# Performance work log

Measured on AMD Instinct MI355X. Metric: run time of the kernel, lower is better.

Reference implementation:

```python
import jax, jax.numpy as jnp
import numpy as np

N_NODES = 50000
N_EDGES = 800000
IN_FEATS = 9
H_FEATS = 64
HEADS = 3
N_CLASSES = 2
NEG_SLOPE = 0.2  # DGL GATConv default leaky_relu slope


def _gat_layer(x, src, dst, W, attn_l, attn_r, bias, n_nodes):
    """One DGL-style GATConv: returns [N, H, F_out] (pre head-sum)."""
    H, Fo = attn_l.shape
    feat = (x @ W).reshape(n_nodes, H, Fo)            # [N,H,Fo]
    el = jnp.einsum('nhf,hf->nh', feat, attn_l)        # [N,H]
    er = jnp.einsum('nhf,hf->nh', feat, attn_r)        # [N,H]
    e = jax.nn.leaky_relu(el[src] + er[dst], negative_slope=NEG_SLOPE)  # [E,H]
    # edge softmax over incoming edges per destination node
    m = jax.ops.segment_max(e, dst, num_segments=n_nodes)               # [N,H]
    ex = jnp.exp(e - m[dst])                                             # [E,H]
    s = jax.ops.segment_sum(ex, dst, num_segments=n_nodes)              # [N,H]
    alpha = ex / s[dst]                                                  # [E,H]
    # attention-weighted neighbor aggregation
    rst = jax.ops.segment_sum(alpha[:, :, None] * feat[src], dst,
                              num_segments=n_nodes)                      # [N,H,Fo]
    return rst + bias.reshape(1, H, Fo)


def setup_inputs() -> dict:
    key = jax.random.key(0)
    ks = jax.random.split(key, 16)
    feats = jax.random.normal(ks[0], (N_NODES, IN_FEATS), dtype=jnp.float32)
    src = jax.random.randint(ks[1], (N_EDGES,), 0, N_NODES, dtype=jnp.int32)
    dst = jax.random.randint(ks[2], (N_EDGES,), 0, N_NODES, dtype=jnp.int32)
    sc = 0.1
    # layer 1: in_feats -> H*H_FEATS
    W1 = jax.random.normal(ks[3], (IN_FEATS, HEADS * H_FEATS), dtype=jnp.float32) * sc
    al1 = jax.random.normal(ks[4], (HEADS, H_FEATS), dtype=jnp.float32) * sc
    ar1 = jax.random.normal(ks[5], (HEADS, H_FEATS), dtype=jnp.float32) * sc
    b1 = jnp.zeros((HEADS * H_FEATS,), dtype=jnp.float32)
    # middle block layer: H_FEATS -> H*H_FEATS
    W2 = jax.random.normal(ks[6], (H_FEATS, HEADS * H_FEATS), dtype=jnp.float32) * sc
    al2 = jax.random.normal(ks[7], (HEADS, H_FEATS), dtype=jnp.float32) * sc
    ar2 = jax.random.normal(ks[8], (HEADS, H_FEATS), dtype=jnp.float32) * sc
    b2 = jnp.zeros((HEADS * H_FEATS,), dtype=jnp.float32)
    # output layer: H_FEATS -> H*N_CLASSES
    W3 = jax.random.normal(ks[9], (H_FEATS, HEADS * N_CLASSES), dtype=jnp.float32) * sc
    al3 = jax.random.normal(ks[10], (HEADS, N_CLASSES), dtype=jnp.float32) * sc
    ar3 = jax.random.normal(ks[11], (HEADS, N_CLASSES), dtype=jnp.float32) * sc
    b3 = jnp.zeros((HEADS * N_CLASSES,), dtype=jnp.float32)
    return {"feats": feats, "src": src, "dst": dst,
            "W1": W1, "al1": al1, "ar1": ar1, "b1": b1,
            "W2": W2, "al2": al2, "ar2": ar2, "b2": b2,
            "W3": W3, "al3": al3, "ar3": ar3, "b3": b3}


def reference(feats, src, dst, W1, al1, ar1, b1, W2, al2, ar2, b2, W3, al3, ar3, b3):
    # dropout layers are identity at inference (in_dropout/feat_drop skipped)
    h = _gat_layer(feats, src, dst, W1, al1, ar1, b1, N_NODES).sum(axis=1)  # [N,H_FEATS]
    h = _gat_layer(h, src, dst, W2, al2, ar2, b2, N_NODES).sum(axis=1)       # [N,H_FEATS]
    o = _gat_layer(h, src, dst, W3, al3, ar3, b3, N_NODES).sum(axis=1)       # [N,N_CLASSES]
    return o
```

## Files before the change

### kernel.cpp

```cpp
#include <hip/hip_runtime.h>
#include <hip/hip_fp16.h>

#define N_NODES 50000
#define N_EDGES 800000
#define NBKT 196
#define BCAP 4480
#define EPB_BIN 4096
#define NB_BIN ((N_EDGES + EPB_BIN - 1) / EPB_BIN)
#define NB_EL 196
#define NB_PW 48

typedef _Float16 half8 __attribute__((ext_vector_type(8)));
typedef float f32x4 __attribute__((ext_vector_type(4)));

static __device__ __forceinline__ float lrelu(float x) { return fmaxf(x, 0.2f * x); }

static __device__ __forceinline__ float2 h2f(float bits) {
    union { float f; __half2 h; } u;
    u.f = bits;
    return __half22float2(u.h);
}
static __device__ __forceinline__ float f2h2(float a, float b) {
    union { float f; __half2 h; } u;
    u.h = __floats2half2_rn(a, b);
    return u.f;
}

__global__ void __launch_bounds__(256) k_front(const int* __restrict__ src,
                                               const int* __restrict__ dst,
                                               int* __restrict__ bfill,
                                               unsigned int* __restrict__ stage,
                                               const float* __restrict__ x,
                                               const float* __restrict__ W1,
                                               const float* __restrict__ al1,
                                               const float* __restrict__ ar1,
                                               float* __restrict__ xph,
                                               float* __restrict__ er,
                                               const float* __restrict__ W2,
                                               __half* __restrict__ Wt16,
                                               const float* __restrict__ al2,
                                               const float* __restrict__ ar2,
                                               float* __restrict__ Wa2,
                                               float* __restrict__ Wr2) {
    __shared__ int lcnt[NBKT];
    __shared__ int gb[NBKT];
    __shared__ int lf[NBKT];
    __shared__ float sWa[9 * 3];
    __shared__ float sWr[9 * 3];
    const int t = threadIdx.x;
    const int b = blockIdx.x;

    if (b < NB_BIN) {
        const int e0 = b * EPB_BIN;
        for (int i = t; i < NBKT; i += 256) lcnt[i] = 0;
        __syncthreads();
        int dcache[16];
#pragma unroll
        for (int i = 0; i < 16; ++i) {
            const int e = e0 + i * 256 + t;
            if (e < N_EDGES) {
                const int d = dst[e];
                dcache[i] = d;
                atomicAdd(&lcnt[d >> 8], 1);
            } else dcache[i] = -1;
        }
        __syncthreads();
        for (int i = t; i < NBKT; i += 256) {
            gb[i] = i * BCAP + atomicAdd(&bfill[i], lcnt[i]);
            lf[i] = 0;
        }
        __syncthreads();
#pragma unroll
        for (int i = 0; i < 16; ++i) {
            const int e = e0 + i * 256 + t;
            if (e < N_EDGES) {
                const int d = dcache[i];
                const int bk = d >> 8;
                const int r = atomicAdd(&lf[bk], 1);
                stage[gb[bk] + r] = (unsigned int)src[e] | ((unsigned int)(d & 255) << 16);
            }
        }
        return;
    }
    if (b < NB_BIN + NB_EL) {
        if (t < 27) {
            const int h = t / 9, k = t % 9;
            float sa = 0.f, sr = 0.f;
            for (int f = 0; f < 64; ++f) {
                const float w = W1[k * 192 + h * 64 + f];
                sa += w * al1[h * 64 + f];
                sr += w * ar1[h * 64 + f];
            }
            sWa[k * 3 + h] = sa;
            sWr[k * 3 + h] = sr;
        }
        __syncthreads();
        const int n = (b - NB_BIN) * 256 + t;
        if (n >= N_NODES) return;
        const float* __restrict__ xr = x + (size_t)n * 9;
        float xv[9];
        float a0 = 0.f, a1 = 0.f, a2 = 0.f, r0 = 0.f, r1 = 0.f, r2 = 0.f;
#pragma unroll
        for (int k = 0; k < 9; ++k) {
            xv[k] = xr[k];
            a0 += xv[k] * sWa[k * 3 + 0];
            a1 += xv[k] * sWa[k * 3 + 1];
            a2 += xv[k] * sWa[k * 3 + 2];
            r0 += xv[k] * sWr[k * 3 + 0];
            r1 += xv[k] * sWr[k * 3 + 1];
            r2 += xv[k] * sWr[k * 3 + 2];
        }
        float* __restrict__ xo = xph + (size_t)n * 8;
        *reinterpret_cast<float4*>(xo) = make_float4(a0, a1, a2, f2h2(xv[0], xv[1]));
        *reinterpret_cast<float4*>(xo + 4) =
            make_float4(f2h2(xv[2], xv[3]), f2h2(xv[4], xv[5]),
                        f2h2(xv[6], xv[7]), f2h2(xv[8], 0.f));
        *reinterpret_cast<float4*>(er + (size_t)n * 4) = make_float4(r0, r1, r2, 0.f);
        return;
    }
    if (b < NB_BIN + NB_EL + NB_PW) {
        const int idx = (b - (NB_BIN + NB_EL)) * 256 + t;
        if (idx < 64 * 192) {
            const int n = idx / 192, ke = idx % 192;
            Wt16[idx] = __float2half(W2[(ke & 63) * 192 + (ke >> 6) * 64 + n]);
        }
        return;
    }
    if (t < 192) {
        const int h = t >> 6, k = t & 63;
        float sa = 0.f, sr = 0.f;
        for (int f = 0; f < 64; ++f) {
            const float w = W2[k * 192 + h * 64 + f];
            sa += w * al2[h * 64 + f];
            sr += w * ar2[h * 64 + f];
        }
        Wa2[k * 4 + h] = sa;
        Wr2[k * 4 + h] = sr;
        if (h == 0) { Wa2[k * 4 + 3] = 0.f; Wr2[k * 4 + 3] = 0.f; }
    }
}

__global__ void __launch_bounds__(512) k_bscatter2(const unsigned int* __restrict__ stage,
                                                   const int* __restrict__ bfill,
                                                   int* __restrict__ rowp,
                                                   int* __restrict__ col) {
    __shared__ int lcnt[256];
    __shared__ int lpos[256];
    __shared__ int sexc[256];
    __shared__ int sscan[256];
    const int t = threadIdx.x;
    const int b = blockIdx.x;
    const int n0 = b << 8;
    int bv = 0;
    if (t < 256) {
        bv = (t < NBKT) ? bfill[t] : 0;
        sscan[t] = bv;
        lcnt[t] = 0;
    }
    __syncthreads();
    for (int off = 1; off < 256; off <<= 1) {
        int u = 0;
        if (t < 256 && t >= off) u = sscan[t - off];
        __syncthreads();
        if (t < 256) sscan[t] += u;
        __syncthreads();
    }
    const int base = (b == 0) ? 0 : sscan[b - 1];
    const int cnt = bfill[b];
    const unsigned int* __restrict__ st = stage + (size_t)b * BCAP;

    for (int j = t; j < cnt; j += 512)
        atomicAdd(&lcnt[(st[j] >> 16) & 255], 1);
    __syncthreads();
    int v = 0;
    if (t < 256) { v = lcnt[t]; lpos[t] = v; }
    __syncthreads();
    for (int off = 1; off < 256; off <<= 1) {
        int u = 0;
        if (t < 256 && t >= off) u = lpos[t - off];
        __syncthreads();
        if (t < 256) lpos[t] += u;
        __syncthreads();
    }
    if (t < 256) {
        sexc[t] = lpos[t] - v;
        if (n0 + t < N_NODES) rowp[n0 + t] = base + sexc[t];
        lcnt[t] = 0;
    }
    if (b == NBKT - 1 && t == 0) rowp[N_NODES] = N_EDGES;
    __syncthreads();
    for (int j = t; j < cnt; j += 512) {
        const unsigned int e = st[j];
        const int local = (int)(e >> 16) & 255;
        const int r = atomicAdd(&lcnt[local], 1);
        col[base + sexc[local] + r] = (int)(e & 0xFFFFu);
    }
}

__global__ void __launch_bounds__(256, 6) k_l1(const float* __restrict__ xph,
                                               const float* __restrict__ er_in,
                                               const int* __restrict__ rowp,
                                               const int* __restrict__ col,
                                               const float* __restrict__ W1,
                                               const float* __restrict__ b1,
                                               const float* __restrict__ Wa2,
                                               const float* __restrict__ Wr2,
                                               __half* __restrict__ hout,
                                               float* __restrict__ el,
                                               float* __restrict__ er_out) {
    __shared__ union {
        float At[16 * 28];
        float vbuf[16][72];
    } u;
    __shared__ float part[3][16][64];
    const int t = threadIdx.x;
    const int wv = t >> 6;
    const int lane = t & 63;
    const int q = lane >> 4;
    const int ql = lane & 15;
    const int li = wv * 4 + q;
    const int nbase = blockIdx.x * 16;
    const int n = nbase + li;
    const char* __restrict__ xb = (const char*)xph;

    {
        const int jb = rowp[n], je = rowp[n + 1];
        const float4 er4 = *reinterpret_cast<const float4*>(er_in + (size_t)n * 4);
        float acc[27];
#pragma unroll
        for (int j = 0; j < 27; ++j) acc[j] = 0.f;
        float sw0 = 0.f, sw1 = 0.f, sw2 = 0.f;

        for (int e = jb + ql; e < je; e += 32) {
            const int e2 = e + 16;
            const bool v2 = (e2 < je);
            const int off1 = col[e] << 5;
            const int off2 = (v2 ? col[e2] : col[e]) << 5;
            const float4 xa1 = *reinterpret_cast<const float4*>(xb + off1);
            const float4 xb1 = *reinterpret_cast<const float4*>(xb + off1 + 16);
            const float4 xa2 = *reinterpret_cast<const float4*>(xb + off2);
            const float4 xb2 = *reinterpret_cast<const float4*>(xb + off2 + 16);
            const float m2 = v2 ? 1.f : 0.f;
            const float w10 = __expf(lrelu(xa1.x + er4.x));
            const float w11 = __expf(lrelu(xa1.y + er4.y));
            const float w12 = __expf(lrelu(xa1.z + er4.z));
            const float w20 = __expf(lrelu(xa2.x + er4.x)) * m2;
            const float w21 = __expf(lrelu(xa2.y + er4.y)) * m2;
            const float w22 = __expf(lrelu(xa2.z + er4.z)) * m2;
            sw0 += w10 + w20; sw1 += w11 + w21; sw2 += w12 + w22;
            const float2 p10 = h2f(xa1.w), p11 = h2f(xb1.x), p12 = h2f(xb1.y),
                         p13 = h2f(xb1.z), p14 = h2f(xb1.w);
            const float2 p20 = h2f(xa2.w), p21 = h2f(xb2.x), p22 = h2f(xb2.y),
                         p23 = h2f(xb2.z), p24 = h2f(xb2.w);
            const float x1[9] = {p10.x, p10.y, p11.x, p11.y, p12.x, p12.y, p13.x, p13.y, p14.x};
            const float x2[9] = {p20.x, p20.y, p21.x, p21.y, p22.x, p22.y, p23.x, p23.y, p24.x};
#pragma unroll
            for (int k = 0; k < 9; ++k) {
                acc[0 + k]  += w10 * x1[k] + w20 * x2[k];
                acc[9 + k]  += w11 * x1[k] + w21 * x2[k];
                acc[18 + k] += w12 * x1[k] + w22 * x2[k];
            }
        }
#pragma unroll
        for (int off = 1; off < 16; off <<= 1) {
            sw0 += __shfl_xor(sw0, off);
            sw1 += __shfl_xor(sw1, off);
            sw2 += __shfl_xor(sw2, off);
#pragma unroll
            for (int j = 0; j < 27; ++j) acc[j] += __shfl_xor(acc[j], off);
        }
        if (ql == 0) {
            const bool has = (je > jb);
            const float i0 = has ? 1.f / sw0 : 0.f;
            const float i1 = has ? 1.f / sw1 : 0.f;
            const float i2 = has ? 1.f / sw2 : 0.f;
            float* __restrict__ ao = u.At + li * 28;
#pragma unroll
            for (int k = 0; k < 9; ++k) {
                ao[k] = acc[k] * i0;
                ao[9 + k] = acc[9 + k] * i1;
                ao[18 + k] = acc[18 + k] * i2;
            }
        }
    }
    __syncthreads();

    {
        const int h = wv;
        const int c = lane;
        if (h < 3) {
            float wreg[9];
#pragma unroll
            for (int k = 0; k < 9; ++k) wreg[k] = W1[k * 192 + h * 64 + c];
#pragma unroll
            for (int i = 0; i < 16; ++i) {
                const float* __restrict__ arp = u.At + i * 28 + h * 9;
                float acc = 0.f;
#pragma unroll
                for (int k = 0; k < 9; ++k) acc += arp[k] * wreg[k];
                part[h][i][c] = acc;
            }
        }
        __syncthreads();
        const float bsum = b1[c] + b1[64 + c] + b1[128 + c];
        for (int idx = t; idx < 1024; idx += 256) {
            const int i = idx >> 6, cc = idx & 63;
            const float v = part[0][i][cc] + part[1][i][cc] + part[2][i][cc] + bsum;
            hout[(size_t)(nbase + i) * 64 + cc] = __float2half(v);
            u.vbuf[i][cc] = v;
        }
        __syncthreads();
        if (t < 96) {
            const int i = t / 6, r = t % 6;
            const int h3 = (r < 3) ? r : r - 3;
            const float* __restrict__ tab = (r < 3) ? Wa2 : Wr2;
            float s = 0.f;
#pragma unroll 8
            for (int c2 = 0; c2 < 64; ++c2) s += u.vbuf[i][c2] * tab[c2 * 4 + h3];
            if (r < 3) el[(size_t)(nbase + i) * 4 + h3] = s;
            else       er_out[(size_t)(nbase + i) * 4 + h3] = s;
        }
    }
}

__global__ void __launch_bounds__(256, 6) k_aggw64(const __half* __restrict__ x,
                                                   const float* __restrict__ el,
                                                   const float* __restrict__ er,
                                                   const int* __restrict__ rowp,
                                                   const int* __restrict__ col,
                                                   __half* __restrict__ agg) {
    const int t = threadIdx.x;
    const int wv = t >> 6;
    const int lane = t & 63;
    const int q = lane >> 4;
    const int ql = lane & 15;
    const int n = (blockIdx.x * 4 + wv) * 4 + q;
    const int jb = rowp[n], je = rowp[n + 1];

    __shared__ float4 wbuf[4][4][16];
    const float4 er4 = *reinterpret_cast<const float4*>(er + (size_t)n * 4);
    const char* __restrict__ xbase = (const char*)x;
    const char* __restrict__ elbase = (const char*)el;
    const int foff = ql * 8;

    float acc[12];
#pragma unroll
    for (int j = 0; j < 12; ++j) acc[j] = 0.f;
    float sw0 = 0.f, sw1 = 0.f, sw2 = 0.f;

    for (int c0 = jb; c0 < je; c0 += 16) {
        const int cnt = min(16, je - c0);
        if (ql < cnt) {
            const int s = col[c0 + ql];
            const float4 e4 = *reinterpret_cast<const float4*>(elbase + (s << 4));
            const float w0 = __expf(lrelu(e4.x + er4.x));
            const float w1 = __expf(lrelu(e4.y + er4.y));
            const float w2 = __expf(lrelu(e4.z + er4.z));
            wbuf[wv][q][ql] = make_float4(w0, w1, w2, __int_as_float(s << 7));
            sw0 += w0; sw1 += w1; sw2 += w2;
        }
        __builtin_amdgcn_wave_barrier();
        int k = 0;
        for (; k + 4 <= cnt; k += 4) {
            const float4 q0 = wbuf[wv][q][k];
            const float4 q1 = wbuf[wv][q][k + 1];
            const float4 q2 = wbuf[wv][q][k + 2];
            const float4 q3 = wbuf[wv][q][k + 3];
            const float2 r0 = *reinterpret_cast<const float2*>(xbase + (__float_as_int(q0.w) + foff));
            const float2 r1 = *reinterpret_cast<const float2*>(xbase + (__float_as_int(q1.w) + foff));
            const float2 r2 = *reinterpret_cast<const float2*>(xbase + (__float_as_int(q2.w) + foff));
            const float2 r3 = *reinterpret_cast<const float2*>(xbase + (__float_as_int(q3.w) + foff));
            const float2 a01 = h2f(r0.x), a23 = h2f(r0.y);
            const float2 b01 = h2f(r1.x), b23 = h2f(r1.y);
            const float2 c01 = h2f(r2.x), c23 = h2f(r2.y);
            const float2 d01 = h2f(r3.x), d23 = h2f(r3.y);
            acc[0] += q0.x * a01.x + q1.x * b01.x + q2.x * c01.x + q3.x * d01.x;
            acc[1] += q0.x * a01.y + q1.x * b01.y + q2.x * c01.y + q3.x * d01.y;
            acc[2] += q0.x * a23.x + q1.x * b23.x + q2.x * c23.x + q3.x * d23.x;
            acc[3] += q0.x * a23.y + q1.x * b23.y + q2.x * c23.y + q3.x * d23.y;
            acc[4] += q0.y * a01.x + q1.y * b01.x + q2.y * c01.x + q3.y * d01.x;
            acc[5] += q0.y * a01.y + q1.y * b01.y + q2.y * c01.y + q3.y * d01.y;
            acc[6] += q0.y * a23.x + q1.y * b23.x + q2.y * c23.x + q3.y * d23.x;
            acc[7] += q0.y * a23.y + q1.y * b23.y + q2.y * c23.y + q3.y * d23.y;
            acc[8]  += q0.z * a01.x + q1.z * b01.x + q2.z * c01.x + q3.z * d01.x;
            acc[9]  += q0.z * a01.y + q1.z * b01.y + q2.z * c01.y + q3.z * d01.y;
            acc[10] += q0.z * a23.x + q1.z * b23.x + q2.z * c23.x + q3.z * d23.x;
            acc[11] += q0.z * a23.y + q1.z * b23.y + q2.z * c23.y + q3.z * d23.y;
        }
        for (; k < cnt; ++k) {
            const float4 q0 = wbuf[wv][q][k];
            const float2 r0 = *reinterpret_cast<const float2*>(xbase + (__float_as_int(q0.w) + foff));
            const float2 a01 = h2f(r0.x), a23 = h2f(r0.y);
            acc[0] += q0.x * a01.x; acc[1] += q0.x * a01.y;
            acc[2] += q0.x * a23.x; acc[3] += q0.x * a23.y;
            acc[4] += q0.y * a01.x; acc[5] += q0.y * a01.y;
            acc[6] += q0.y * a23.x; acc[7] += q0.y * a23.y;
            acc[8]  += q0.z * a01.x; acc[9]  += q0.z * a01.y;
            acc[10] += q0.z * a23.x; acc[11] += q0.z * a23.y;
        }
    }
#pragma unroll
    for (int off = 1; off < 16; off <<= 1) {
        sw0 += __shfl_xor(sw0, off);
        sw1 += __shfl_xor(sw1, off);
        sw2 += __shfl_xor(sw2, off);
    }
    {
        __half* __restrict__ ao = agg + (size_t)n * 192 + ql * 4;
        if (je > jb) {
            const float i0 = 1.f / sw0, i1 = 1.f / sw1, i2 = 1.f / sw2;
            *reinterpret_cast<float2*>(ao) =
                make_float2(f2h2(acc[0] * i0, acc[1] * i0), f2h2(acc[2] * i0, acc[3] * i0));
            *reinterpret_cast<float2*>(ao + 64) =
                make_float2(f2h2(acc[4] * i1, acc[5] * i1), f2h2(acc[6] * i1, acc[7] * i1));
            *reinterpret_cast<float2*>(ao + 128) =
                make_float2(f2h2(acc[8] * i2, acc[9] * i2), f2h2(acc[10] * i2, acc[11] * i2));
        } else {
            const float2 z = make_float2(f2h2(0.f, 0.f), f2h2(0.f, 0.f));
            *reinterpret_cast<float2*>(ao) = z;
            *reinterpret_cast<float2*>(ao + 64) = z;
            *reinterpret_cast<float2*>(ao + 128) = z;
        }
    }
}

__global__ void __launch_bounds__(256) k_l23(const __half* __restrict__ aggH,
                                             const __half* __restrict__ Wt,
                                             const float* __restrict__ b2,
                                             const float* __restrict__ W3,
                                             const float* __restrict__ al3,
                                             const float* __restrict__ ar3,
                                             float* __restrict__ feat3p,
                                             float* __restrict__ er3) {
    __shared__ float xl[64 * 68];
    __shared__ float Wl[64 * 6];
    __shared__ float Wal[64 * 3];
    __shared__ float Wrl[64 * 3];
    const int t = threadIdx.x;
    const int n0 = blockIdx.x * 64;
    const int nvalid = min(64, N_NODES - n0);

    {
        const int wv = t >> 6;
        const int lane = t & 63;
        const int quad = lane >> 4;
        const int t16 = lane & 15;
        const int nwave = n0 + wv * 16;
        const int arow = min(nwave + t16, N_NODES - 1);
        half8 a[6];
#pragma unroll
        for (int kb = 0; kb < 6; ++kb)
            a[kb] = *reinterpret_cast<const half8*>(aggH + (size_t)arow * 192 + kb * 32 + quad * 8);
#pragma unroll
        for (int nt = 0; nt < 4; ++nt) {
            const int c = nt * 16 + t16;
            const float bs = b2[c] + b2[64 + c] + b2[128 + c];
            const __half* __restrict__ bt = Wt + (size_t)c * 192 + quad * 8;
            f32x4 acc = {0.f, 0.f, 0.f, 0.f};
#pragma unroll
            for (int kb = 0; kb < 6; ++kb) {
                const half8 bfr = *reinterpret_cast<const half8*>(bt + kb * 32);
                acc = __builtin_amdgcn_mfma_f32_16x16x32_f16(a[kb], bfr, acc, 0, 0, 0);
            }
#pragma unroll
            for (int r = 0; r < 4; ++r)
                xl[(wv * 16 + quad * 4 + r) * 68 + c] = acc[r] + bs;
        }
    }
    for (int idx = t; idx < 384; idx += 256) Wl[idx] = W3[idx];
    if (t < 192) {
        const int k = t & 63, h = t >> 6;
        Wal[k * 3 + h] = W3[k * 6 + h * 2] * al3[h * 2] + W3[k * 6 + h * 2 + 1] * al3[h * 2 + 1];
        Wrl[k * 3 + h] = W3[k * 6 + h * 2] * ar3[h * 2] + W3[k * 6 + h * 2 + 1] * ar3[h * 2 + 1];
    }
    __syncthreads();

#pragma unroll
    for (int hp = 0; hp < 2; ++hp) {
        const int i = (t >> 3) + hp * 32;
        const int slot = t & 7;
        if (i < nvalid && slot < 6) {
            float acc = 0.f;
#pragma unroll
            for (int k4 = 0; k4 < 16; ++k4) {
                const float4 xv = *reinterpret_cast<const float4*>(&xl[i * 68 + 4 * k4]);
                acc += Wl[(4 * k4 + 0) * 6 + slot] * xv.x;
                acc += Wl[(4 * k4 + 1) * 6 + slot] * xv.y;
                acc += Wl[(4 * k4 + 2) * 6 + slot] * xv.z;
                acc += Wl[(4 * k4 + 3) * 6 + slot] * xv.w;
            }
            reinterpret_cast<__half*>(feat3p + (size_t)(n0 + i) * 8)[6 + slot] = __float2half(acc);
        }
        if (t < 192) {
            const int ii = t / 6 + hp * 32, ss = t % 6;
            if (ii < nvalid) {
                const int hh = (ss < 3) ? ss : ss - 3;
                const float* __restrict__ wt = (ss < 3) ? Wal : Wrl;
                float acc = 0.f;
#pragma unroll 4
                for (int k = 0; k < 64; ++k) acc += xl[ii * 68 + k] * wt[k * 3 + hh];
                if (ss < 3) feat3p[(size_t)(n0 + ii) * 8 + hh] = acc;
                else        er3[(size_t)(n0 + ii) * 4 + hh] = acc;
            }
        }
    }
}

__global__ void __launch_bounds__(256, 4) k_agg3(const float* __restrict__ feat3p,
                                                 const float* __restrict__ er3,
                                                 const float* __restrict__ b3,
                                                 const int* __restrict__ rowp,
                                                 const int* __restrict__ col,
                                                 float* __restrict__ out) {
    const int tid = threadIdx.x;
    const int wv = tid >> 6;
    const int lane = tid & 63;
    const int q = lane >> 4;
    const int ql = lane & 15;
    const int n = (blockIdx.x * 4 + wv) * 4 + q;
    const int jb = rowp[n], je = rowp[n + 1];
    const float4 er4 = *reinterpret_cast<const float4*>(er3 + (size_t)n * 4);
    const char* __restrict__ fb = (const char*)feat3p;

    float acc[6];
#pragma unroll
    for (int j = 0; j < 6; ++j) acc[j] = 0.f;
    float sw0 = 0.f, sw1 = 0.f, sw2 = 0.f;

    for (int e = jb + ql; e < je; e += 64) {
        const int eb = e + 16, ec = e + 32, ed = e + 48;
        const bool vb = (eb < je), vc = (ec < je), vd = (ed < je);
        const int sa = col[e];
        const int offa = sa << 5;
        const int offb = (vb ? col[eb] : sa) << 5;
        const int offc = (vc ? col[ec] : sa) << 5;
        const int offd = (vd ? col[ed] : sa) << 5;
        const float4 fa1 = *reinterpret_cast<const float4*>(fb + offa);
        const float2 fb1 = *reinterpret_cast<const float2*>(fb + offa + 16);
        const float4 fa2 = *reinterpret_cast<const float4*>(fb + offb);
        const float2 fb2 = *reinterpret_cast<const float2*>(fb + offb + 16);
        const float4 fa3 = *reinterpret_cast<const float4*>(fb + offc);
        const float2 fb3 = *reinterpret_cast<const float2*>(fb + offc + 16);
        const float4 fa4 = *reinterpret_cast<const float4*>(fb + offd);
        const float2 fb4 = *reinterpret_cast<const float2*>(fb + offd + 16);
        const float mb = vb ? 1.f : 0.f, mc = vc ? 1.f : 0.f, md = vd ? 1.f : 0.f;
        const float w10 = __expf(lrelu(fa1.x + er4.x));
        const float w11 = __expf(lrelu(fa1.y + er4.y));
        const float w12 = __expf(lrelu(fa1.z + er4.z));
        const float w20 = __expf(lrelu(fa2.x + er4.x)) * mb;
        const float w21 = __expf(lrelu(fa2.y + er4.y)) * mb;
        const float w22 = __expf(lrelu(fa2.z + er4.z)) * mb;
        const float w30 = __expf(lrelu(fa3.x + er4.x)) * mc;
        const float w31 = __expf(lrelu(fa3.y + er4.y)) * mc;
        const float w32 = __expf(lrelu(fa3.z + er4.z)) * mc;
        const float w40 = __expf(lrelu(fa4.x + er4.x)) * md;
        const float w41 = __expf(lrelu(fa4.y + er4.y)) * md;
        const float w42 = __expf(lrelu(fa4.z + er4.z)) * md;
        sw0 += (w10 + w20) + (w30 + w40);
        sw1 += (w11 + w21) + (w31 + w41);
        sw2 += (w12 + w22) + (w32 + w42);
        const float2 f01a = h2f(fa1.w), f23a = h2f(fb1.x), f45a = h2f(fb1.y);
        const float2 f01b = h2f(fa2.w), f23b = h2f(fb2.x), f45b = h2f(fb2.y);
        const float2 f01c = h2f(fa3.w), f23c = h2f(fb3.x), f45c = h2f(fb3.y);
        const float2 f01d = h2f(fa4.w), f23d = h2f(fb4.x), f45d = h2f(fb4.y);
        acc[0] += (w10 * f01a.x + w20 * f01b.x) + (w30 * f01c.x + w40 * f01d.x);
        acc[1] += (w10 * f01a.y + w20 * f01b.y) + (w30 * f01c.y + w40 * f01d.y);
        acc[2] += (w11 * f23a.x + w21 * f23b.x) + (w31 * f23c.x + w41 * f23d.x);
        acc[3] += (w11 * f23a.y + w21 * f23b.y) + (w31 * f23c.y + w41 * f23d.y);
        acc[4] += (w12 * f45a.x + w22 * f45b.x) + (w32 * f45c.x + w42 * f45d.x);
        acc[5] += (w12 * f45a.y + w22 * f45b.y) + (w32 * f45c.y + w42 * f45d.y);
    }
#pragma unroll
    for (int off = 1; off < 16; off <<= 1) {
        sw0 += __shfl_xor(sw0, off);
        sw1 += __shfl_xor(sw1, off);
        sw2 += __shfl_xor(sw2, off);
#pragma unroll
        for (int j = 0; j < 6; ++j) acc[j] += __shfl_xor(acc[j], off);
    }
    if (ql == 0) {
        const bool has = (je > jb);
        const float i0 = has ? 1.f / sw0 : 0.f;
        const float i1 = has ? 1.f / sw1 : 0.f;
        const float i2 = has ? 1.f / sw2 : 0.f;
        const float o0 = acc[0] * i0 + acc[2] * i1 + acc[4] * i2 + b3[0] + b3[2] + b3[4];
        const float o1 = acc[1] * i0 + acc[3] * i1 + acc[5] * i2 + b3[1] + b3[3] + b3[5];
        *reinterpret_cast<float2*>(out + (size_t)n * 2) = make_float2(o0, o1);
    }
}

extern "C" void kernel_launch(void* const* d_in, const int* in_sizes, int n_in,
                              void* d_out, int out_size, void* d_ws, size_t ws_size,
                              hipStream_t stream) {
    const float* feats = (const float*)d_in[0];
    const int* src = (const int*)d_in[1];
    const int* dst = (const int*)d_in[2];
    const float* W1 = (const float*)d_in[3];
    const float* al1 = (const float*)d_in[4];
    const float* ar1 = (const float*)d_in[5];
    const float* b1 = (const float*)d_in[6];
    const float* W2 = (const float*)d_in[7];
    const float* al2 = (const float*)d_in[8];
    const float* ar2 = (const float*)d_in[9];
    const float* b2 = (const float*)d_in[10];
    const float* W3 = (const float*)d_in[11];
    const float* al3 = (const float*)d_in[12];
    const float* ar3 = (const float*)d_in[13];
    const float* b3 = (const float*)d_in[14];
    float* out = (float*)d_out;

    char* ws = (char*)d_ws;
    size_t off = 0;
    auto alloc = [&](size_t bytes) {
        void* p = ws + off;
        off += (bytes + 255) & ~(size_t)255;
        return p;
    };
    __half* aggH = (__half*)alloc((size_t)N_NODES * 192 * 2);
    __half* hbufH = (__half*)alloc((size_t)N_NODES * 64 * 2);
    float* xph = (float*)alloc((size_t)N_NODES * 8 * 4);
    float* el = (float*)alloc((size_t)N_NODES * 4 * 4);
    float* er = (float*)alloc((size_t)N_NODES * 4 * 4);
    int* bfill = (int*)alloc(256 * 4);
    int* rowp = (int*)alloc((size_t)(N_NODES + 1) * 4);
    int* col = (int*)alloc((size_t)N_EDGES * 4);
    unsigned int* stage = (unsigned int*)alloc((size_t)NBKT * BCAP * 4);
    __half* Wt16 = (__half*)alloc((size_t)64 * 192 * 2);
    float* Wa2 = (float*)alloc(256 * 4);
    float* Wr2 = (float*)alloc(256 * 4);
    float* feat3p = (float*)alloc((size_t)N_NODES * 8 * 4);
    (void)ws_size;

    const int qb = N_NODES / 16;
    const int lb = (N_NODES + 63) / 64;

    hipMemsetAsync(bfill, 0, 256 * 4, stream);
    k_front<<<NB_BIN + NB_EL + NB_PW + 1, 256, 0, stream>>>(
        src, dst, bfill, stage, feats, W1, al1, ar1, xph, er, W2, Wt16,
        al2, ar2, Wa2, Wr2);
    k_bscatter2<<<NBKT, 512, 0, stream>>>(stage, bfill, rowp, col);

    k_l1<<<qb, 256, 0, stream>>>(xph, er, rowp, col, W1, b1, Wa2, Wr2, hbufH, el, er);

    k_aggw64<<<qb, 256, 0, stream>>>(hbufH, el, er, rowp, col, aggH);

    k_l23<<<lb, 256, 0, stream>>>(aggH, Wt16, b2, W3, al3, ar3, feat3p, er);

    k_agg3<<<qb, 256, 0, stream>>>(feat3p, er, b3, rowp, col, out);
}
```

Measured before the change: 202.9 us.

## Remap layer-1 and layer-3 aggregation to four lanes per node, wave-local

In k_l1 and k_agg3, each destination node is now handled by 4 lanes instead of 16, so one wave covers 16 nodes and a block covers 64. Average degree is about 16, so this is meant to cut idle lanes and shuffle-reduction steps. k_l1's dense projection and el/er epilogue now run per wave, with each wave summing its three heads in registers, so block-wide __syncthreads are replaced by wave barriers. The cost is more shared memory and registers per block in k_l1, which now has a lower occupancy bound, and a serial loop for high-degree nodes.

```diff
diff --git a/kernel.cpp b/kernel.cpp
--- a/kernel.cpp
+++ b/kernel.cpp
@@ -197,7 +197,7 @@
     }
 }
 
-__global__ void __launch_bounds__(256, 6) k_l1(const float* __restrict__ xph,
+__global__ void __launch_bounds__(256, 4) k_l1(const float* __restrict__ xph,
                                                const float* __restrict__ er_in,
                                                const int* __restrict__ rowp,
                                                const int* __restrict__ col,
@@ -208,31 +208,30 @@
                                                __half* __restrict__ hout,
                                                float* __restrict__ el,
                                                float* __restrict__ er_out) {
-    __shared__ union {
-        float At[16 * 28];
-        float vbuf[16][72];
-    } u;
-    __shared__ float part[3][16][64];
+    __shared__ float At[4][16][28];
+    __shared__ float vbuf[4][16][72];
     const int t = threadIdx.x;
     const int wv = t >> 6;
     const int lane = t & 63;
-    const int q = lane >> 4;
-    const int ql = lane & 15;
-    const int li = wv * 4 + q;
-    const int nbase = blockIdx.x * 16;
-    const int n = nbase + li;
+    const int i16 = lane >> 2;
+    const int j = lane & 3;
+    const int nbase = blockIdx.x * 64 + wv * 16;
+    const int n = nbase + i16;
+    const bool valid = (n < N_NODES);
     const char* __restrict__ xb = (const char*)xph;
 
     {
-        const int jb = rowp[n], je = rowp[n + 1];
-        const float4 er4 = *reinterpret_cast<const float4*>(er_in + (size_t)n * 4);
+        const int jb = valid ? rowp[n] : 0;
+        const int je = valid ? rowp[n + 1] : 0;
+        const float4 er4 = valid ? *reinterpret_cast<const float4*>(er_in + (size_t)n * 4)
+                                 : make_float4(0.f, 0.f, 0.f, 0.f);
         float acc[27];
 #pragma unroll
-        for (int j = 0; j < 27; ++j) acc[j] = 0.f;
+        for (int k = 0; k < 27; ++k) acc[k] = 0.f;
         float sw0 = 0.f, sw1 = 0.f, sw2 = 0.f;
 
-        for (int e = jb + ql; e < je; e += 32) {
-            const int e2 = e + 16;
+        for (int e = jb + j; e < je; e += 8) {
+            const int e2 = e + 4;
             const bool v2 = (e2 < je);
             const int off1 = col[e] << 5;
             const int off2 = (v2 ? col[e2] : col[e]) << 5;
@@ -262,19 +261,19 @@
             }
         }
 #pragma unroll
-        for (int off = 1; off < 16; off <<= 1) {
+        for (int off = 1; off < 4; off <<= 1) {
             sw0 += __shfl_xor(sw0, off);
             sw1 += __shfl_xor(sw1, off);
             sw2 += __shfl_xor(sw2, off);
 #pragma unroll
-            for (int j = 0; j < 27; ++j) acc[j] += __shfl_xor(acc[j], off);
-        }
-        if (ql == 0) {
+            for (int k = 0; k < 27; ++k) acc[k] += __shfl_xor(acc[k], off);
+        }
+        if (j == 0) {
             const bool has = (je > jb);
             const float i0 = has ? 1.f / sw0 : 0.f;
             const float i1 = has ? 1.f / sw1 : 0.f;
             const float i2 = has ? 1.f / sw2 : 0.f;
-            float* __restrict__ ao = u.At + li * 28;
+            float* __restrict__ ao = At[wv][i16];
 #pragma unroll
             for (int k = 0; k < 9; ++k) {
                 ao[k] = acc[k] * i0;
@@ -283,42 +282,49 @@
             }
         }
     }
-    __syncthreads();
+    __builtin_amdgcn_wave_barrier();
 
     {
-        const int h = wv;
         const int c = lane;
-        if (h < 3) {
+        float hid[16];
+#pragma unroll
+        for (int i = 0; i < 16; ++i) hid[i] = 0.f;
+#pragma unroll
+        for (int h = 0; h < 3; ++h) {
             float wreg[9];
 #pragma unroll
             for (int k = 0; k < 9; ++k) wreg[k] = W1[k * 192 + h * 64 + c];
 #pragma unroll
             for (int i = 0; i < 16; ++i) {
-                const float* __restrict__ arp = u.At + i * 28 + h * 9;
-                float acc = 0.f;
-#pragma unroll
-                for (int k = 0; k < 9; ++k) acc += arp[k] * wreg[k];
-                part[h][i][c] = acc;
-            }
-        }
-        __syncthreads();
+                const float* __restrict__ arp = At[wv][i] + h * 9;
+                float a = 0.f;
+#pragma unroll
+                for (int k = 0; k < 9; ++k) a += arp[k] * wreg[k];
+                hid[i] += a;
+            }
+        }
         const float bsum = b1[c] + b1[64 + c] + b1[128 + c];
-        for (int idx = t; idx < 1024; idx += 256) {
-            const int i = idx >> 6, cc = idx & 63;
-            const float v = part[0][i][cc] + part[1][i][cc] + part[2][i][cc] + bsum;
-            hout[(size_t)(nbase + i) * 64 + cc] = __float2half(v);
-            u.vbuf[i][cc] = v;
-        }
-        __syncthreads();
-        if (t < 96) {
-            const int i = t / 6, r = t % 6;
-            const int h3 = (r < 3) ? r : r - 3;
-            const float* __restrict__ tab = (r < 3) ? Wa2 : Wr2;
-            float s = 0.f;
+#pragma unroll
+        for (int i = 0; i < 16; ++i) {
+            const int ni = nbase + i;
+            const float v = hid[i] + bsum;
+            if (ni < N_NODES) hout[(size_t)ni * 64 + c] = __float2half(v);
+            vbuf[wv][i][c] = v;
+        }
+    }
+    __builtin_amdgcn_wave_barrier();
+
+    for (int o = lane; o < 96; o += 64) {
+        const int i = o / 6, r = o % 6;
+        const int ni = nbase + i;
+        const int h3 = (r < 3) ? r : r - 3;
+        const float* __restrict__ tab = (r < 3) ? Wa2 : Wr2;
+        float s = 0.f;
 #pragma unroll 8
-            for (int c2 = 0; c2 < 64; ++c2) s += u.vbuf[i][c2] * tab[c2 * 4 + h3];
-            if (r < 3) el[(size_t)(nbase + i) * 4 + h3] = s;
-            else       er_out[(size_t)(nbase + i) * 4 + h3] = s;
+        for (int c2 = 0; c2 < 64; ++c2) s += vbuf[wv][i][c2] * tab[c2 * 4 + h3];
+        if (ni < N_NODES) {
+            if (r < 3) el[(size_t)ni * 4 + h3] = s;
+            else       er_out[(size_t)ni * 4 + h3] = s;
         }
     }
 }
@@ -506,79 +512,64 @@
     }
 }
 
-__global__ void __launch_bounds__(256, 4) k_agg3(const float* __restrict__ feat3p,
+__global__ void __launch_bounds__(256, 8) k_agg3(const float* __restrict__ feat3p,
                                                  const float* __restrict__ er3,
                                                  const float* __restrict__ b3,
                                                  const int* __restrict__ rowp,
                                                  const int* __restrict__ col,
                                                  float* __restrict__ out) {
-    const int tid = threadIdx.x;
-    const int wv = tid >> 6;
-    const int lane = tid & 63;
-    const int q = lane >> 4;
-    const int ql = lane & 15;
-    const int n = (blockIdx.x * 4 + wv) * 4 + q;
-    const int jb = rowp[n], je = rowp[n + 1];
-    const float4 er4 = *reinterpret_cast<const float4*>(er3 + (size_t)n * 4);
+    const int t = threadIdx.x;
+    const int lane = t & 63;
+    const int i16 = lane >> 2;
+    const int j = lane & 3;
+    const int n = blockIdx.x * 64 + (t >> 6) * 16 + i16;
+    const bool valid = (n < N_NODES);
+    const int jb = valid ? rowp[n] : 0;
+    const int je = valid ? rowp[n + 1] : 0;
+    const float4 er4 = valid ? *reinterpret_cast<const float4*>(er3 + (size_t)n * 4)
+                             : make_float4(0.f, 0.f, 0.f, 0.f);
     const char* __restrict__ fb = (const char*)feat3p;
 
     float acc[6];
 #pragma unroll
-    for (int j = 0; j < 6; ++j) acc[j] = 0.f;
+    for (int k = 0; k < 6; ++k) acc[k] = 0.f;
     float sw0 = 0.f, sw1 = 0.f, sw2 = 0.f;
 
-    for (int e = jb + ql; e < je; e += 64) {
-        const int eb = e + 16, ec = e + 32, ed = e + 48;
-        const bool vb = (eb < je), vc = (ec < je), vd = (ed < je);
-        const int sa = col[e];
-        const int offa = sa << 5;
-        const int offb = (vb ? col[eb] : sa) << 5;
-        const int offc = (vc ? col[ec] : sa) << 5;
-        const int offd = (vd ? col[ed] : sa) << 5;
+    for (int e = jb + j; e < je; e += 8) {
+        const int e2 = e + 4;
+        const bool v2 = (e2 < je);
+        const int offa = col[e] << 5;
+        const int offb = (v2 ? col[e2] : col[e]) << 5;
         const float4 fa1 = *reinterpret_cast<const float4*>(fb + offa);
         const float2 fb1 = *reinterpret_cast<const float2*>(fb + offa + 16);
         const float4 fa2 = *reinterpret_cast<const float4*>(fb + offb);
         const float2 fb2 = *reinterpret_cast<const float2*>(fb + offb + 16);
-        const float4 fa3 = *reinterpret_cast<const float4*>(fb + offc);
-        const float2 fb3 = *reinterpret_cast<const float2*>(fb + offc + 16);
-        const float4 fa4 = *reinterpret_cast<const float4*>(fb + offd);
-        const float2 fb4 = *reinterpret_cast<const float2*>(fb + offd + 16);
-        const float mb = vb ? 1.f : 0.f, mc = vc ? 1.f : 0.f, md = vd ? 1.f : 0.f;
+        const float m2 = v2 ? 1.f : 0.f;
         const float w10 = __expf(lrelu(fa1.x + er4.x));
         const float w11 = __expf(lrelu(fa1.y + er4.y));
         const float w12 = __expf(lrelu(fa1.z + er4.z));
-        const float w20 = __expf(lrelu(fa2.x + er4.x)) * mb;
-        const float w21 = __expf(lrelu(fa2.y + er4.y)) * mb;
-        const float w22 = __expf(lrelu(fa2.z + er4.z)) * mb;
-        const float w30 = __expf(lrelu(fa3.x + er4.x)) * mc;
-        const float w31 = __expf(lrelu(fa3.y + er4.y)) * mc;
-        const float w32 = __expf(lrelu(fa3.z + er4.z)) * mc;
-        const float w40 = __expf(lrelu(fa4.x + er4.x)) * md;
-        const float w41 = __expf(lrelu(fa4.y + er4.y)) * md;
-        const float w42 = __expf(lrelu(fa4.z + er4.z)) * md;
-        sw0 += (w10 + w20) + (w30 + w40);
-        sw1 += (w11 + w21) + (w31 + w41);
-        sw2 += (w12 + w22) + (w32 + w42);
+        const float w20 = __expf(lrelu(fa2.x + er4.x)) * m2;
+        const float w21 = __expf(lrelu(fa2.y + er4.y)) * m2;
+        const float w22 = __expf(lrelu(fa2.z + er4.z)) * m2;
+        sw0 += w10 + w20; sw1 += w11 + w21; sw2 += w12 + w22;
         const float2 f01a = h2f(fa1.w), f23a = h2f(fb1.x), f45a = h2f(fb1.y);
         const float2 f01b = h2f(fa2.w), f23b = h2f(fb2.x), f45b = h2f(fb2.y);
-        const float2 f01c = h2f(fa3.w), f23c = h2f(fb3.x), f45c = h2f(fb3.y);
-        const float2 f01d = h2f(fa4.w), f23d = h2f(fb4.x), f45d = h2f(fb4.y);
-        acc[0] += (w10 * f01a.x + w20 * f01b.x) + (w30 * f01c.x + w40 * f01d.x);
-        acc[1] += (w10 * f01a.y + w20 * f01b.y) + (w30 * f01c.y + w40 * f01d.y);
-        acc[2] += (w11 * f23a.x + w21 * f23b.x) + (w31 * f23c.x + w41 * f23d.x);
-        acc[3] += (w11 * f23a.y + w21 * f23b.y) + (w31 * f23c.y + w41 * f23d.y);
-        acc[4] += (w12 * f45a.x + w22 * f45b.x) + (w32 * f45c.x + w42 * f45d.x);
-        acc[5] += (w12 * f45a.y + w22 * f45b.y) + (w32 * f45c.y + w42 * f45d.y);
-    }
-#pragma unroll
-    for (int off = 1; off < 16; off <<= 1) {
+        acc[0] += w10 * f01a.x + w20 * f01b.x;
+        acc[1] += w10 * f01a.y + w20 * f01b.y;
+        acc[2] += w11 * f23a.x + w21 * f23b.x;
+        acc[3] += w11 * f23a.y + w21 * f23b.y;
+        acc[4] += w12 * f45a.x + w22 * f45b.x;
+        acc[5] += w12 * f45a.y + w22 * f45b.y;
+    }
+#pragma unroll
+    for (int off = 1; off < 4; off <<= 1) {
         sw0 += __shfl_xor(sw0, off);
         sw1 += __shfl_xor(sw1, off);
         sw2 += __shfl_xor(sw2, off);
 #pragma unroll
-        for (int j = 0; j < 6; ++j) acc[j] += __shfl_xor(acc[j], off);
-    }
-    if (ql == 0) {
+        for (int k = 0; k < 6; ++k) acc[k] += __shfl_xor(acc[k], off);
+    }
+    if (j == 0 && valid) {
         const bool has = (je > jb);
         const float i0 = has ? 1.f / sw0 : 0.f;
         const float i1 = has ? 1.f / sw1 : 0.f;
@@ -632,7 +623,7 @@
     (void)ws_size;
 
     const int qb = N_NODES / 16;
-    const int lb = (N_NODES + 63) / 64;
+    const int nb64 = (N_NODES + 63) / 64;
 
     hipMemsetAsync(bfill, 0, 256 * 4, stream);
     k_front<<<NB_BIN + NB_EL + NB_PW + 1, 256, 0, stream>>>(
@@ -640,11 +631,11 @@
         al2, ar2, Wa2, Wr2);
     k_bscatter2<<<NBKT, 512, 0, stream>>>(stage, bfill, rowp, col);
 
-    k_l1<<<qb, 256, 0, stream>>>(xph, er, rowp, col, W1, b1, Wa2, Wr2, hbufH, el, er);
+    k_l1<<<nb64, 256, 0, stream>>>(xph, er, rowp, col, W1, b1, Wa2, Wr2, hbufH, el, er);
 
     k_aggw64<<<qb, 256, 0, stream>>>(hbufH, el, er, rowp, col, aggH);
 
-    k_l23<<<lb, 256, 0, stream>>>(aggH, Wt16, b2, W3, al3, ar3, feat3p, er);
-
-    k_agg3<<<qb, 256, 0, stream>>>(feat3p, er, b3, rowp, col, out);
-}
+    k_l23<<<nb64, 256, 0, stream>>>(aggH, Wt16, b2, W3, al3, ar3, feat3p, er);
+
+    k_agg3<<<nb64, 256, 0, stream>>>(feat3p, er, b3, rowp, col, out);
+}
```

After: 327.3 us. +61.3%, slower.

## Remap final aggregation to four lanes per node instead of sixteen

Applied to the files above, without the earlier changes.

The layer-3 aggregation kernel now assigns 4 lanes per destination node (16 nodes per wave) rather than 16 lanes, with 2-way unrolling instead of 4-way. Launch bounds rise to 8 blocks per SM, and the grid is sized by 64 nodes per block with a bounds check. With about 16 edges per node on average, this is meant to cut idle lanes and shuffle-reduction steps. In exchange each lane walks a longer serial edge chain and has fewer loads in flight.

```diff
diff --git a/kernel.cpp b/kernel.cpp
--- a/kernel.cpp
+++ b/kernel.cpp
@@ -506,79 +506,64 @@
     }
 }
 
-__global__ void __launch_bounds__(256, 4) k_agg3(const float* __restrict__ feat3p,
+__global__ void __launch_bounds__(256, 8) k_agg3(const float* __restrict__ feat3p,
                                                  const float* __restrict__ er3,
                                                  const float* __restrict__ b3,
                                                  const int* __restrict__ rowp,
                                                  const int* __restrict__ col,
                                                  float* __restrict__ out) {
-    const int tid = threadIdx.x;
-    const int wv = tid >> 6;
-    const int lane = tid & 63;
-    const int q = lane >> 4;
-    const int ql = lane & 15;
-    const int n = (blockIdx.x * 4 + wv) * 4 + q;
-    const int jb = rowp[n], je = rowp[n + 1];
-    const float4 er4 = *reinterpret_cast<const float4*>(er3 + (size_t)n * 4);
+    const int t = threadIdx.x;
+    const int lane = t & 63;
+    const int i16 = lane >> 2;
+    const int j = lane & 3;
+    const int n = blockIdx.x * 64 + (t >> 6) * 16 + i16;
+    const bool valid = (n < N_NODES);
+    const int jb = valid ? rowp[n] : 0;
+    const int je = valid ? rowp[n + 1] : 0;
+    const float4 er4 = valid ? *reinterpret_cast<const float4*>(er3 + (size_t)n * 4)
+                             : make_float4(0.f, 0.f, 0.f, 0.f);
     const char* __restrict__ fb = (const char*)feat3p;
 
     float acc[6];
 #pragma unroll
-    for (int j = 0; j < 6; ++j) acc[j] = 0.f;
+    for (int k = 0; k < 6; ++k) acc[k] = 0.f;
     float sw0 = 0.f, sw1 = 0.f, sw2 = 0.f;
 
-    for (int e = jb + ql; e < je; e += 64) {
-        const int eb = e + 16, ec = e + 32, ed = e + 48;
-        const bool vb = (eb < je), vc = (ec < je), vd = (ed < je);
-        const int sa = col[e];
-        const int offa = sa << 5;
-        const int offb = (vb ? col[eb] : sa) << 5;
-        const int offc = (vc ? col[ec] : sa) << 5;
-        const int offd = (vd ? col[ed] : sa) << 5;
+    for (int e = jb + j; e < je; e += 8) {
+        const int e2 = e + 4;
+        const bool v2 = (e2 < je);
+        const int offa = col[e] << 5;
+        const int offb = (v2 ? col[e2] : col[e]) << 5;
         const float4 fa1 = *reinterpret_cast<const float4*>(fb + offa);
         const float2 fb1 = *reinterpret_cast<const float2*>(fb + offa + 16);
         const float4 fa2 = *reinterpret_cast<const float4*>(fb + offb);
         const float2 fb2 = *reinterpret_cast<const float2*>(fb + offb + 16);
-        const float4 fa3 = *reinterpret_cast<const float4*>(fb + offc);
-        const float2 fb3 = *reinterpret_cast<const float2*>(fb + offc + 16);
-        const float4 fa4 = *reinterpret_cast<const float4*>(fb + offd);
-        const float2 fb4 = *reinterpret_cast<const float2*>(fb + offd + 16);
-        const float mb = vb ? 1.f : 0.f, mc = vc ? 1.f : 0.f, md = vd ? 1.f : 0.f;
+        const float m2 = v2 ? 1.f : 0.f;
         const float w10 = __expf(lrelu(fa1.x + er4.x));
         const float w11 = __expf(lrelu(fa1.y + er4.y));
         const float w12 = __expf(lrelu(fa1.z + er4.z));
-        const float w20 = __expf(lrelu(fa2.x + er4.x)) * mb;
-        const float w21 = __expf(lrelu(fa2.y + er4.y)) * mb;
-        const float w22 = __expf(lrelu(fa2.z + er4.z)) * mb;
-        const float w30 = __expf(lrelu(fa3.x + er4.x)) * mc;
-        const float w31 = __expf(lrelu(fa3.y + er4.y)) * mc;
-        const float w32 = __expf(lrelu(fa3.z + er4.z)) * mc;
-        const float w40 = __expf(lrelu(fa4.x + er4.x)) * md;
-        const float w41 = __expf(lrelu(fa4.y + er4.y)) * md;
-        const float w42 = __expf(lrelu(fa4.z + er4.z)) * md;
-        sw0 += (w10 + w20) + (w30 + w40);
-        sw1 += (w11 + w21) + (w31 + w41);
-        sw2 += (w12 + w22) + (w32 + w42);
+        const float w20 = __expf(lrelu(fa2.x + er4.x)) * m2;
+        const float w21 = __expf(lrelu(fa2.y + er4.y)) * m2;
+        const float w22 = __expf(lrelu(fa2.z + er4.z)) * m2;
+        sw0 += w10 + w20; sw1 += w11 + w21; sw2 += w12 + w22;
         const float2 f01a = h2f(fa1.w), f23a = h2f(fb1.x), f45a = h2f(fb1.y);
         const float2 f01b = h2f(fa2.w), f23b = h2f(fb2.x), f45b = h2f(fb2.y);
-        const float2 f01c = h2f(fa3.w), f23c = h2f(fb3.x), f45c = h2f(fb3.y);
-        const float2 f01d = h2f(fa4.w), f23d = h2f(fb4.x), f45d = h2f(fb4.y);
-        acc[0] += (w10 * f01a.x + w20 * f01b.x) + (w30 * f01c.x + w40 * f01d.x);
-        acc[1] += (w10 * f01a.y + w20 * f01b.y) + (w30 * f01c.y + w40 * f01d.y);
-        acc[2] += (w11 * f23a.x + w21 * f23b.x) + (w31 * f23c.x + w41 * f23d.x);
-        acc[3] += (w11 * f23a.y + w21 * f23b.y) + (w31 * f23c.y + w41 * f23d.y);
-        acc[4] += (w12 * f45a.x + w22 * f45b.x) + (w32 * f45c.x + w42 * f45d.x);
-        acc[5] += (w12 * f45a.y + w22 * f45b.y) + (w32 * f45c.y + w42 * f45d.y);
-    }
-#pragma unroll
-    for (int off = 1; off < 16; off <<= 1) {
+        acc[0] += w10 * f01a.x + w20 * f01b.x;
+        acc[1] += w10 * f01a.y + w20 * f01b.y;
+        acc[2] += w11 * f23a.x + w21 * f23b.x;
+        acc[3] += w11 * f23a.y + w21 * f23b.y;
+        acc[4] += w12 * f45a.x + w22 * f45b.x;
+        acc[5] += w12 * f45a.y + w22 * f45b.y;
+    }
+#pragma unroll
+    for (int off = 1; off < 4; off <<= 1) {
         sw0 += __shfl_xor(sw0, off);
         sw1 += __shfl_xor(sw1, off);
         sw2 += __shfl_xor(sw2, off);
 #pragma unroll
-        for (int j = 0; j < 6; ++j) acc[j] += __shfl_xor(acc[j], off);
-    }
-    if (ql == 0) {
+        for (int k = 0; k < 6; ++k) acc[k] += __shfl_xor(acc[k], off);
+    }
+    if (j == 0 && valid) {
         const bool has = (je > jb);
         const float i0 = has ? 1.f / sw0 : 0.f;
         const float i1 = has ? 1.f / sw1 : 0.f;
@@ -632,7 +617,7 @@
     (void)ws_size;
 
     const int qb = N_NODES / 16;
-    const int lb = (N_NODES + 63) / 64;
+    const int nb64 = (N_NODES + 63) / 64;
 
     hipMemsetAsync(bfill, 0, 256 * 4, stream);
     k_front<<<NB_BIN + NB_EL + NB_PW + 1, 256, 0, stream>>>(
@@ -644,7 +629,7 @@
 
     k_aggw64<<<qb, 256, 0, stream>>>(hbufH, el, er, rowp, col, aggH);
 
-    k_l23<<<lb, 256, 0, stream>>>(aggH, Wt16, b2, W3, al3, ar3, feat3p, er);
-
-    k_agg3<<<qb, 256, 0, stream>>>(feat3p, er, b3, rowp, col, out);
-}
+    k_l23<<<nb64, 256, 0, stream>>>(aggH, Wt16, b2, W3, al3, ar3, feat3p, er);
+
+    k_agg3<<<nb64, 256, 0, stream>>>(feat3p, er, b3, rowp, col, out);
+}
```

After: 200.4 us. About the same (-1.2%).
